# Performance work log

Measured on AMD Instinct MI355X. Metric: run time of the kernel, lower is better.

The kernel has to match this reference:

```python
import jax, jax.numpy as jnp
import numpy as np

NUM_CODES = 4096
TEMPERATURE = 1.0
EPS = 1e-08


def setup_inputs() -> dict:
    key = jax.random.key(0)
    k1, k2, k3 = jax.random.split(key, 3)
    B, D, T = 16, 512, 1500
    encoder_stride = 320
    student_features = jax.random.normal(k1, (B, D, T), dtype=jnp.float32)
    codebook = jax.random.normal(k2, (NUM_CODES, D), dtype=jnp.float32)
    lengths = jax.random.randint(k3, (B,), 0, T * encoder_stride, dtype=jnp.int64)
    return {
        "student_features": student_features,
        "codebook": codebook,
        "lengths": lengths,
        "encoder_stride": encoder_stride,
    }


def _length_mask(lengths, T, stride):
    # frame t is valid iff t < floor(length / stride)  -> (B, T) float mask
    n_valid = jnp.minimum(lengths // stride, T)
    return (jnp.arange(T)[None, :] < n_valid[:, None]).astype(jnp.float32)


def reference(student_features, codebook, lengths, encoder_stride):
    B, D, T = student_features.shape
    mask = _length_mask(lengths, T, encoder_stride)            # (B, T)
    z = jnp.transpose(student_features, (0, 2, 1)).reshape(-1, D)  # (N, D), N = B*T
    # Euclidean cdist via ||z||^2 + ||c||^2 - 2 z c^T (same as torch.cdist GEMM path)
    z2 = jnp.sum(z * z, axis=-1, keepdims=True)                # (N, 1)
    c2 = jnp.sum(codebook * codebook, axis=-1)                 # (K,)
    d2 = z2 + c2[None, :] - 2.0 * (z @ codebook.T)             # (N, K)
    distances = jnp.sqrt(jnp.maximum(d2, 1e-12))
    logits = -distances / TEMPERATURE
    probs = jax.nn.softmax(logits, axis=-1)                    # (N, K)
    probs_masked = probs * mask.reshape(-1, 1)
    code_dist = jnp.sum(probs_masked, axis=0)                  # (K,)
    code_dist = code_dist / (jnp.sum(code_dist) + EPS)
    entropy = -jnp.sum(code_dist * jnp.log(code_dist + EPS))
    max_entropy = jnp.log(jnp.float32(NUM_CODES))
    return 1.0 - entropy / max_entropy
```

## Files before the change

kernel.cpp:

```cpp
#include <hip/hip_runtime.h>
#include <hip/hip_bf16.h>

#define NUM_B   16
#define DIM     512
#define TT      1500
#define NROWS   (NUM_B * TT)
#define NCODES  4096
#define ROW_TILES ((NROWS + 127) / 128)
#define NROWS_PAD (ROW_TILES * 128)
#define NSLICE  8
#define SHIFTC  30.0f

typedef __bf16 bf16x8 __attribute__((ext_vector_type(8)));
typedef float  floatx4 __attribute__((ext_vector_type(4)));
typedef unsigned short ushortx8 __attribute__((ext_vector_type(8)));

__device__ __forceinline__ void glds16(const void* g, void* l) {
    __builtin_amdgcn_global_load_lds(
        (__attribute__((address_space(1))) void*)(void*)g,
        (__attribute__((address_space(3))) void*)l, 16, 0, 0);
}

__global__ __launch_bounds__(256) void k_transpose(
    const float* __restrict__ sf, unsigned short* __restrict__ zbf,
    float* __restrict__ z2) {
    __shared__ float tile[32][68];
    int tid = threadIdx.x;
    int b = blockIdx.z, d0 = blockIdx.y * 64, t0 = blockIdx.x * 32;
    int tl = tid & 31, dg = tid >> 5;
#pragma unroll
    for (int dd = 0; dd < 8; ++dd) {
        int d = dd * 8 + dg;
        int t = t0 + tl;
        if (t < TT) tile[tl][d] = sf[(size_t)(b * DIM + d0 + d) * TT + t];
    }
    __syncthreads();
    int t = tid >> 3, dgrp = tid & 7;
    int tglob = t0 + t;
    float ssq = 0.f;
    if (tglob < TT) {
        unsigned int h[8];
#pragma unroll
        for (int i = 0; i < 8; ++i) {
            __hip_bfloat16 hb = __float2bfloat16(tile[t][dgrp * 8 + i]);
            h[i] = __builtin_bit_cast(unsigned short, hb);
            float vb = __bfloat162float(hb);
            ssq += vb * vb;
        }
        uint4 o;
        o.x = h[0] | (h[1] << 16); o.y = h[2] | (h[3] << 16);
        o.z = h[4] | (h[5] << 16); o.w = h[6] | (h[7] << 16);
        *(uint4*)(zbf + (size_t)(b * TT + tglob) * DIM + d0 + dgrp * 8) = o;
    }
    ssq += __shfl_xor(ssq, 1); ssq += __shfl_xor(ssq, 2); ssq += __shfl_xor(ssq, 4);
    if (dgrp == 0 && tglob < TT) atomicAdd(&z2[b * TT + tglob], ssq);
}

__global__ void k_cb(const float* __restrict__ cb, unsigned short* __restrict__ cbbf,
                     float* __restrict__ c2) {
    int k = blockIdx.x * 4 + (threadIdx.x >> 6);
    int lane = threadIdx.x & 63;
    const float4* src = (const float4*)(cb + (size_t)k * DIM + lane * 8);
    float4 a = src[0], b2 = src[1];
    float vals[8] = {a.x, a.y, a.z, a.w, b2.x, b2.y, b2.z, b2.w};
    float s = 0.f;
    unsigned int h[8];
#pragma unroll
    for (int i = 0; i < 8; ++i) {
        __hip_bfloat16 hb = __float2bfloat16(vals[i]);
        h[i] = __builtin_bit_cast(unsigned short, hb);
        float vb = __bfloat162float(hb);
        s += vb * vb;
    }
    uint4 o;
    o.x = h[0] | (h[1] << 16); o.y = h[2] | (h[3] << 16);
    o.z = h[4] | (h[5] << 16); o.w = h[6] | (h[7] << 16);
    *(uint4*)(cbbf + (size_t)k * DIM + lane * 8) = o;
#pragma unroll
    for (int off = 32; off >= 1; off >>= 1) s += __shfl_down(s, off);
    if (lane == 0) c2[k] = s;
}

__global__ __launch_bounds__(256, 2) void k_gemm1(
    const unsigned short* __restrict__ zbf, const unsigned short* __restrict__ cbbf,
    const float* __restrict__ z2, const float* __restrict__ c2,
    const int* __restrict__ lengths, const int* __restrict__ stride_p,
    float* __restrict__ Sg, unsigned short* __restrict__ Eg) {
    __shared__ unsigned short As[128 * 64];
    __shared__ unsigned short Bs[128 * 64];
    __shared__ float z2s[128], c2s[128];
    __shared__ unsigned char vldp[128];
    __shared__ int s_any;
    int tid = threadIdx.x;
    int r0 = blockIdx.y * 128, c0 = blockIdx.x * 128;
    if (tid == 0) s_any = 0;
    __syncthreads();
    if (tid < 128) {
        int n = r0 + tid;
        int valid = 0;
        if (n < NROWS) {
            int b = n / TT, t = n - b * TT;
            int stride = stride_p[0];
            int nv = lengths[b] / stride;
            if (nv > TT) nv = TT;
            valid = (t < nv);
        }
        if (valid) atomicOr(&s_any, 1);
        vldp[tid] = (unsigned char)valid;
        z2s[tid] = z2[r0 + tid];
        c2s[tid] = c2[c0 + tid];
    }
    __syncthreads();
    if (!s_any) return;

    int wave = tid >> 6, lane = tid & 63;
    int l15 = lane & 15, l4 = lane >> 4;
    int wr = (wave >> 1) * 64, wc = (wave & 1) * 64;

    int srow = lane >> 3;
    int scg = (lane & 7) ^ srow;
    const unsigned short* ag = zbf + (size_t)(r0 + wave * 32 + srow) * DIM + scg * 8;
    const unsigned short* bg = cbbf + (size_t)(c0 + wave * 32 + srow) * DIM + scg * 8;
    unsigned short* al = As + (wave * 32) * 64;
    unsigned short* bl = Bs + (wave * 32) * 64;

    floatx4 acc[4][4];
    const floatx4 zero = {0.f, 0.f, 0.f, 0.f};
#pragma unroll
    for (int i = 0; i < 4; ++i)
#pragma unroll
        for (int j = 0; j < 4; ++j) acc[i][j] = zero;

    int sw = l15 & 7;

    for (int kc = 0; kc < 8; ++kc) {
#pragma unroll
        for (int q = 0; q < 4; ++q) {
            glds16(ag + (size_t)q * 8 * DIM + kc * 64, al + q * 8 * 64);
            glds16(bg + (size_t)q * 8 * DIM + kc * 64, bl + q * 8 * 64);
        }
        __syncthreads();
#pragma unroll
        for (int ks = 0; ks < 64; ks += 32) {
            int g = (ks >> 3) + l4;
            int pcg = g ^ sw;
            bf16x8 av[4], bv[4];
#pragma unroll
            for (int i = 0; i < 4; ++i)
                av[i] = __builtin_bit_cast(bf16x8,
                    *(const ushortx8*)&As[(wr + 16 * i + l15) * 64 + pcg * 8]);
#pragma unroll
            for (int j = 0; j < 4; ++j)
                bv[j] = __builtin_bit_cast(bf16x8,
                    *(const ushortx8*)&Bs[(wc + 16 * j + l15) * 64 + pcg * 8]);
#pragma unroll
            for (int i = 0; i < 4; ++i)
#pragma unroll
                for (int j = 0; j < 4; ++j)
                    acc[i][j] = __builtin_amdgcn_mfma_f32_16x16x32_bf16(av[i], bv[j], acc[i][j], 0, 0, 0);
        }
        __syncthreads();
    }

#pragma unroll
    for (int i = 0; i < 4; ++i) {
#pragma unroll
        for (int r = 0; r < 4; ++r) {
            int rl = wr + 16 * i + 4 * l4 + r;
            bool rv = vldp[rl] != 0;
            float z2v = z2s[rl];
            float s = 0.f;
            unsigned short* Ep = Eg + (size_t)(r0 + rl) * NCODES + c0 + wc + l15;
#pragma unroll
            for (int j = 0; j < 4; ++j) {
                int cl = wc + 16 * j + l15;
                float d2 = z2v + c2s[cl] - 2.0f * acc[i][j][r];
                float d = sqrtf(fmaxf(d2, 1e-12f));
                float e = __expf(SHIFTC - d);
                s += e;
                if (rv) Ep[16 * j] = __builtin_bit_cast(unsigned short, __float2bfloat16(e));
            }
            s += __shfl_xor(s, 1); s += __shfl_xor(s, 2);
            s += __shfl_xor(s, 4); s += __shfl_xor(s, 8);
            if (l15 == 0 && rv) atomicAdd(&Sg[r0 + rl], s);
        }
    }
}

__global__ __launch_bounds__(256) void k_scan(
    const unsigned short* __restrict__ Eg, const float* __restrict__ Sg,
    const int* __restrict__ lengths, const int* __restrict__ stride_p,
    float* __restrict__ cdp) {
    __shared__ float rs[32];
    __shared__ int s_any;
    int tid = threadIdx.x;
    int r0 = blockIdx.y * 32;
    if (tid == 0) s_any = 0;
    __syncthreads();
    if (tid < 32) {
        int n = r0 + tid;
        int valid = 0;
        if (n < NROWS) {
            int b = n / TT, t = n - b * TT;
            int nv = lengths[b] / stride_p[0];
            if (nv > TT) nv = TT;
            valid = (t < nv);
        }
        if (valid) atomicOr(&s_any, 1);
        rs[tid] = valid ? 1.0f / Sg[n] : 0.0f;
    }
    __syncthreads();
    if (!s_any) return;

    int col0 = blockIdx.x * 2048 + tid * 8;
    float acc[8] = {0.f, 0.f, 0.f, 0.f, 0.f, 0.f, 0.f, 0.f};
    for (int nn = 0; nn < 32; ++nn) {
        float rn = rs[nn];
        if (rn == 0.f) continue;
        uint4 v = *(const uint4*)(Eg + (size_t)(r0 + nn) * NCODES + col0);
        unsigned int u[4] = {v.x, v.y, v.z, v.w};
#pragma unroll
        for (int q = 0; q < 4; ++q) {
            acc[2 * q]     += rn * __builtin_bit_cast(float, u[q] << 16);
            acc[2 * q + 1] += rn * __builtin_bit_cast(float, u[q] & 0xffff0000u);
        }
    }
    float* outp = cdp + (size_t)(blockIdx.y & (NSLICE - 1)) * NCODES;
#pragma unroll
    for (int t = 0; t < 8; ++t) atomicAdd(&outp[col0 + t], acc[t]);
}

template <int PASS>
__global__ __launch_bounds__(256, 2) void k_gemm(
    const unsigned short* __restrict__ zbf, const unsigned short* __restrict__ cbbf,
    const float* __restrict__ z2, const float* __restrict__ c2,
    const int* __restrict__ lengths, const int* __restrict__ stride_p,
    float* __restrict__ Sg, float* __restrict__ cd) {
    __shared__ unsigned short As[128 * 64];
    __shared__ unsigned short Bs[128 * 64];
    __shared__ float z2s[128], c2s[128], rs[128];
    __shared__ int s_any;
    int tid = threadIdx.x;
    int r0 = blockIdx.y * 128, c0 = blockIdx.x * 128;
    if (tid == 0) s_any = 0;
    __syncthreads();
    if (tid < 128) {
        int n = r0 + tid;
        int valid = 0;
        if (n < NROWS) {
            int b = n / TT, t = n - b * TT;
            int stride = stride_p[0];
            int nv = lengths[b] / stride;
            if (nv > TT) nv = TT;
            valid = (t < nv);
        }
        if (valid) atomicOr(&s_any, 1);
        z2s[tid] = z2[r0 + tid];
        c2s[tid] = c2[c0 + tid];
        if (PASS == 2) rs[tid] = valid ? (1.0f / Sg[r0 + tid]) : 0.0f;
    }
    __syncthreads();
    if (!s_any) return;

    int wave = tid >> 6, lane = tid & 63;
    int l15 = lane & 15, l4 = lane >> 4;
    int wr = (wave >> 1) * 64, wc = (wave & 1) * 64;
    int srow = lane >> 3;
    int scg = (lane & 7) ^ srow;
    const unsigned short* ag = zbf + (size_t)(r0 + wave * 32 + srow) * DIM + scg * 8;
    const unsigned short* bg = cbbf + (size_t)(c0 + wave * 32 + srow) * DIM + scg * 8;
    unsigned short* al = As + (wave * 32) * 64;
    unsigned short* bl = Bs + (wave * 32) * 64;

    floatx4 acc[4][4];
    const floatx4 zero = {0.f, 0.f, 0.f, 0.f};
#pragma unroll
    for (int i = 0; i < 4; ++i)
#pragma unroll
        for (int j = 0; j < 4; ++j) acc[i][j] = zero;
    int sw = l15 & 7;
    for (int kc = 0; kc < 8; ++kc) {
#pragma unroll
        for (int q = 0; q < 4; ++q) {
            glds16(ag + (size_t)q * 8 * DIM + kc * 64, al + q * 8 * 64);
            glds16(bg + (size_t)q * 8 * DIM + kc * 64, bl + q * 8 * 64);
        }
        __syncthreads();
#pragma unroll
        for (int ks = 0; ks < 64; ks += 32) {
            int g = (ks >> 3) + l4;
            int pcg = g ^ sw;
            bf16x8 av[4], bv[4];
#pragma unroll
            for (int i = 0; i < 4; ++i)
                av[i] = __builtin_bit_cast(bf16x8, *(const ushortx8*)&As[(wr + 16 * i + l15) * 64 + pcg * 8]);
#pragma unroll
            for (int j = 0; j < 4; ++j)
                bv[j] = __builtin_bit_cast(bf16x8, *(const ushortx8*)&Bs[(wc + 16 * j + l15) * 64 + pcg * 8]);
#pragma unroll
            for (int i = 0; i < 4; ++i)
#pragma unroll
                for (int j = 0; j < 4; ++j)
                    acc[i][j] = __builtin_amdgcn_mfma_f32_16x16x32_bf16(av[i], bv[j], acc[i][j], 0, 0, 0);
        }
        __syncthreads();
    }
    if (PASS == 1) {
#pragma unroll
        for (int i = 0; i < 4; ++i) {
#pragma unroll
            for (int r = 0; r < 4; ++r) {
                int rl = wr + 16 * i + 4 * l4 + r;
                float z2v = z2s[rl];
                float s = 0.f;
#pragma unroll
                for (int j = 0; j < 4; ++j) {
                    int cl = wc + 16 * j + l15;
                    float d2 = z2v + c2s[cl] - 2.0f * acc[i][j][r];
                    float d = sqrtf(fmaxf(d2, 1e-12f));
                    s += __expf(SHIFTC - d);
                }
                s += __shfl_xor(s, 1); s += __shfl_xor(s, 2);
                s += __shfl_xor(s, 4); s += __shfl_xor(s, 8);
                if (l15 == 0) atomicAdd(&Sg[r0 + rl], s);
            }
        }
    } else {
#pragma unroll
        for (int j = 0; j < 4; ++j) {
            int cl = wc + 16 * j + l15;
            float c2v = c2s[cl];
            float cs = 0.f;
#pragma unroll
            for (int i = 0; i < 4; ++i) {
#pragma unroll
                for (int r = 0; r < 4; ++r) {
                    int rl = wr + 16 * i + 4 * l4 + r;
                    float d2 = z2s[rl] + c2v - 2.0f * acc[i][j][r];
                    float d = sqrtf(fmaxf(d2, 1e-12f));
                    cs += __expf(SHIFTC - d) * rs[rl];
                }
            }
            cs += __shfl_xor(cs, 16); cs += __shfl_xor(cs, 32);
            if (l4 == 0) atomicAdd(&cd[c0 + cl], cs);
        }
    }
}

__global__ __launch_bounds__(1024) void k_final(const float* __restrict__ cdp,
                                                float* __restrict__ out) {
    __shared__ float red[16];
    __shared__ float tot_s;
    int tid = threadIdx.x, lane = tid & 63, wave = tid >> 6;
    float vloc[4];
    float t = 0.f;
#pragma unroll
    for (int q = 0; q < 4; ++q) {
        int i = tid + q * 1024;
        float v = 0.f;
#pragma unroll
        for (int s = 0; s < NSLICE; ++s) v += cdp[(size_t)s * NCODES + i];
        vloc[q] = v;
        t += v;
    }
#pragma unroll
    for (int off = 32; off >= 1; off >>= 1) t += __shfl_down(t, off);
    if (lane == 0) red[wave] = t;
    __syncthreads();
    if (tid == 0) {
        float tt = 0.f;
#pragma unroll
        for (int w = 0; w < 16; ++w) tt += red[w];
        tot_s = tt;
    }
    __syncthreads();
    float inv = 1.0f / (tot_s + 1e-8f);
    float e = 0.f;
#pragma unroll
    for (int q = 0; q < 4; ++q) {
        float p = vloc[q] * inv;
        e += p * __logf(p + 1e-8f);
    }
#pragma unroll
    for (int off = 32; off >= 1; off >>= 1) e += __shfl_down(e, off);
    if (lane == 0) red[wave] = e;
    __syncthreads();
    if (tid == 0) {
        float ee = 0.f;
#pragma unroll
        for (int w = 0; w < 16; ++w) ee += red[w];
        out[0] = 1.0f - (-ee) / __logf((float)NCODES);
    }
}

extern "C" void kernel_launch(void* const* d_in, const int* in_sizes, int n_in,
                              void* d_out, int out_size, void* d_ws, size_t ws_size,
                              hipStream_t stream) {
    const float* sf = (const float*)d_in[0];
    const float* cb = (const float*)d_in[1];
    const int* lengths = (const int*)d_in[2];
    const int* stride_p = (const int*)d_in[3];

    float* Sg = (float*)d_ws;
    float* cdp = Sg + NROWS_PAD;
    float* z2 = cdp + (size_t)NSLICE * NCODES;
    float* c2 = z2 + NROWS_PAD;
    unsigned short* zbf = (unsigned short*)(c2 + NCODES);
    unsigned short* cbbf = zbf + (size_t)NROWS_PAD * DIM;
    unsigned short* Eg = cbbf + (size_t)NCODES * DIM;

    size_t base_bytes = (size_t)(2 * NROWS_PAD + NCODES) * 4
                      + (size_t)NSLICE * NCODES * 4
                      + ((size_t)NROWS_PAD * DIM + (size_t)NCODES * DIM) * 2;
    size_t need = base_bytes + (size_t)NROWS_PAD * NCODES * 2;

    hipMemsetAsync(Sg, 0, ((size_t)2 * NROWS_PAD + (size_t)NSLICE * NCODES) * sizeof(float), stream);
    k_transpose<<<dim3((TT + 31) / 32, DIM / 64, NUM_B), 256, 0, stream>>>(sf, zbf, z2);
    k_cb<<<dim3(NCODES / 4), 256, 0, stream>>>(cb, cbbf, c2);
    if (ws_size >= need) {
        k_gemm1<<<dim3(NCODES / 128, ROW_TILES), 256, 0, stream>>>(zbf, cbbf, z2, c2, lengths, stride_p, Sg, Eg);
        k_scan<<<dim3(NCODES / 2048, NROWS_PAD / 32), 256, 0, stream>>>(Eg, Sg, lengths, stride_p, cdp);
    } else {
        k_gemm<1><<<dim3(NCODES / 128, ROW_TILES), 256, 0, stream>>>(zbf, cbbf, z2, c2, lengths, stride_p, Sg, cdp);
        k_gemm<2><<<dim3(NCODES / 128, ROW_TILES), 256, 0, stream>>>(zbf, cbbf, z2, c2, lengths, stride_p, Sg, cdp);
    }
    k_final<<<1, 1024, 0, stream>>>(cdp, (float*)d_out);
}
```

Before: 236.4 us.

## Fuse prep kernels, memset, scan and final reduction into fewer launches

Merges the transpose, codebook conversion and workspace zeroing into a single prep kernel, using a full-D shared tile so z2 is written directly instead of accumulated atomically. The GEMM kernel now has the last block per row tile do the column-sum scan of that tile, and the last block overall compute the entropy. This replaces the separate scan and final kernels via atomic counters. It aims to cut launch overhead and memsets, but it serialises the scan work onto one block per row tile and adds a large 32x513 shared tile that may lower occupancy in the prep kernel.

New measurement: 745.7 us. +215.4%, slower.

```diff
diff --git a/kernel.cpp b/kernel.cpp
--- a/kernel.cpp
+++ b/kernel.cpp
@@ -10,6 +10,11 @@
 #define NROWS_PAD (ROW_TILES * 128)
 #define NSLICE  8
 #define SHIFTC  30.0f
+#define NBLKX   (NCODES / 128)
+#define NBLK    (NBLKX * ROW_TILES)
+#define TBLKS   (NUM_B * 47)
+#define CBLKS   (NCODES / 4)
+#define NZERO   (NROWS_PAD + NSLICE * NCODES + ROW_TILES + 1)
 
 typedef __bf16 bf16x8 __attribute__((ext_vector_type(8)));
 typedef float  floatx4 __attribute__((ext_vector_type(4)));
@@ -21,76 +26,90 @@
         (__attribute__((address_space(3))) void*)l, 16, 0, 0);
 }
 
-__global__ __launch_bounds__(256) void k_transpose(
-    const float* __restrict__ sf, unsigned short* __restrict__ zbf,
-    float* __restrict__ z2) {
-    __shared__ float tile[32][68];
-    int tid = threadIdx.x;
-    int b = blockIdx.z, d0 = blockIdx.y * 64, t0 = blockIdx.x * 32;
-    int tl = tid & 31, dg = tid >> 5;
-#pragma unroll
-    for (int dd = 0; dd < 8; ++dd) {
-        int d = dd * 8 + dg;
+__global__ __launch_bounds__(256) void k_prep(
+    const float* __restrict__ sf, const float* __restrict__ cb,
+    unsigned short* __restrict__ zbf, unsigned short* __restrict__ cbbf,
+    float* __restrict__ z2, float* __restrict__ c2, float* __restrict__ zero0) {
+    int id = blockIdx.x, tid = threadIdx.x;
+    if (id < TBLKS) {
+        __shared__ float tile[32][513];
+        int b = id / 47, t0 = (id % 47) * 32;
+        int tl = tid & 31, dg = tid >> 5;
         int t = t0 + tl;
-        if (t < TT) tile[tl][d] = sf[(size_t)(b * DIM + d0 + d) * TT + t];
-    }
-    __syncthreads();
-    int t = tid >> 3, dgrp = tid & 7;
-    int tglob = t0 + t;
-    float ssq = 0.f;
-    if (tglob < TT) {
+        if (t < TT) {
+            const float* src = sf + (size_t)b * DIM * TT + t;
+#pragma unroll 8
+            for (int k = 0; k < 64; ++k) {
+                int d = dg * 64 + k;
+                tile[tl][d] = src[(size_t)d * TT];
+            }
+        }
+        __syncthreads();
+        int tr = tid >> 3, dgr = tid & 7;
+        int tg = t0 + tr;
+        float ssq = 0.f;
+        if (tg < TT) {
+            unsigned short* dst = zbf + (size_t)(b * TT + tg) * DIM;
+#pragma unroll
+            for (int seg = 0; seg < 8; ++seg) {
+                int d0 = seg * 64 + dgr * 8;
+                unsigned int h[8];
+#pragma unroll
+                for (int i2 = 0; i2 < 8; ++i2) {
+                    __hip_bfloat16 hb = __float2bfloat16(tile[tr][d0 + i2]);
+                    h[i2] = __builtin_bit_cast(unsigned short, hb);
+                    float vb = __bfloat162float(hb);
+                    ssq += vb * vb;
+                }
+                uint4 o;
+                o.x = h[0] | (h[1] << 16); o.y = h[2] | (h[3] << 16);
+                o.z = h[4] | (h[5] << 16); o.w = h[6] | (h[7] << 16);
+                *(uint4*)(dst + d0) = o;
+            }
+        }
+        ssq += __shfl_xor(ssq, 1); ssq += __shfl_xor(ssq, 2); ssq += __shfl_xor(ssq, 4);
+        if (dgr == 0 && tg < TT) z2[b * TT + tg] = ssq;
+    } else {
+        int ci = id - TBLKS;
+        int gid = ci * 256 + tid;
+        if (gid < NZERO) zero0[gid] = 0.f;
+        int k = ci * 4 + (tid >> 6);
+        int lane = tid & 63;
+        const float4* src = (const float4*)(cb + (size_t)k * DIM + lane * 8);
+        float4 a = src[0], b2 = src[1];
+        float vals[8] = {a.x, a.y, a.z, a.w, b2.x, b2.y, b2.z, b2.w};
+        float s = 0.f;
         unsigned int h[8];
 #pragma unroll
         for (int i = 0; i < 8; ++i) {
-            __hip_bfloat16 hb = __float2bfloat16(tile[t][dgrp * 8 + i]);
+            __hip_bfloat16 hb = __float2bfloat16(vals[i]);
             h[i] = __builtin_bit_cast(unsigned short, hb);
             float vb = __bfloat162float(hb);
-            ssq += vb * vb;
+            s += vb * vb;
         }
         uint4 o;
         o.x = h[0] | (h[1] << 16); o.y = h[2] | (h[3] << 16);
         o.z = h[4] | (h[5] << 16); o.w = h[6] | (h[7] << 16);
-        *(uint4*)(zbf + (size_t)(b * TT + tglob) * DIM + d0 + dgrp * 8) = o;
-    }
-    ssq += __shfl_xor(ssq, 1); ssq += __shfl_xor(ssq, 2); ssq += __shfl_xor(ssq, 4);
-    if (dgrp == 0 && tglob < TT) atomicAdd(&z2[b * TT + tglob], ssq);
-}
-
-__global__ void k_cb(const float* __restrict__ cb, unsigned short* __restrict__ cbbf,
-                     float* __restrict__ c2) {
-    int k = blockIdx.x * 4 + (threadIdx.x >> 6);
-    int lane = threadIdx.x & 63;
-    const float4* src = (const float4*)(cb + (size_t)k * DIM + lane * 8);
-    float4 a = src[0], b2 = src[1];
-    float vals[8] = {a.x, a.y, a.z, a.w, b2.x, b2.y, b2.z, b2.w};
-    float s = 0.f;
-    unsigned int h[8];
-#pragma unroll
-    for (int i = 0; i < 8; ++i) {
-        __hip_bfloat16 hb = __float2bfloat16(vals[i]);
-        h[i] = __builtin_bit_cast(unsigned short, hb);
-        float vb = __bfloat162float(hb);
-        s += vb * vb;
-    }
-    uint4 o;
-    o.x = h[0] | (h[1] << 16); o.y = h[2] | (h[3] << 16);
-    o.z = h[4] | (h[5] << 16); o.w = h[6] | (h[7] << 16);
-    *(uint4*)(cbbf + (size_t)k * DIM + lane * 8) = o;
-#pragma unroll
-    for (int off = 32; off >= 1; off >>= 1) s += __shfl_down(s, off);
-    if (lane == 0) c2[k] = s;
+        *(uint4*)(cbbf + (size_t)k * DIM + lane * 8) = o;
+#pragma unroll
+        for (int off = 32; off >= 1; off >>= 1) s += __shfl_down(s, off);
+        if (lane == 0) c2[k] = s;
+    }
 }
 
 __global__ __launch_bounds__(256, 2) void k_gemm1(
     const unsigned short* __restrict__ zbf, const unsigned short* __restrict__ cbbf,
     const float* __restrict__ z2, const float* __restrict__ c2,
     const int* __restrict__ lengths, const int* __restrict__ stride_p,
-    float* __restrict__ Sg, unsigned short* __restrict__ Eg) {
+    float* __restrict__ Sg, unsigned short* __restrict__ Eg,
+    float* __restrict__ cdp, int* __restrict__ rowcnt, int* __restrict__ blockdone,
+    float* __restrict__ out) {
     __shared__ unsigned short As[128 * 64];
     __shared__ unsigned short Bs[128 * 64];
-    __shared__ float z2s[128], c2s[128];
+    __shared__ float z2s[128], c2s[128], rsS[128];
     __shared__ unsigned char vldp[128];
-    __shared__ int s_any;
+    __shared__ int s_any, sh_e;
+    __shared__ float red[4], tot_s;
     int tid = threadIdx.x;
     int r0 = blockIdx.y * 128, c0 = blockIdx.x * 128;
     if (tid == 0) s_any = 0;
@@ -111,123 +130,146 @@
         c2s[tid] = c2[c0 + tid];
     }
     __syncthreads();
-    if (!s_any) return;
-
-    int wave = tid >> 6, lane = tid & 63;
-    int l15 = lane & 15, l4 = lane >> 4;
-    int wr = (wave >> 1) * 64, wc = (wave & 1) * 64;
-
-    int srow = lane >> 3;
-    int scg = (lane & 7) ^ srow;
-    const unsigned short* ag = zbf + (size_t)(r0 + wave * 32 + srow) * DIM + scg * 8;
-    const unsigned short* bg = cbbf + (size_t)(c0 + wave * 32 + srow) * DIM + scg * 8;
-    unsigned short* al = As + (wave * 32) * 64;
-    unsigned short* bl = Bs + (wave * 32) * 64;
-
-    floatx4 acc[4][4];
-    const floatx4 zero = {0.f, 0.f, 0.f, 0.f};
-#pragma unroll
-    for (int i = 0; i < 4; ++i)
-#pragma unroll
-        for (int j = 0; j < 4; ++j) acc[i][j] = zero;
-
-    int sw = l15 & 7;
-
-    for (int kc = 0; kc < 8; ++kc) {
-#pragma unroll
-        for (int q = 0; q < 4; ++q) {
-            glds16(ag + (size_t)q * 8 * DIM + kc * 64, al + q * 8 * 64);
-            glds16(bg + (size_t)q * 8 * DIM + kc * 64, bl + q * 8 * 64);
-        }
-        __syncthreads();
-#pragma unroll
-        for (int ks = 0; ks < 64; ks += 32) {
-            int g = (ks >> 3) + l4;
-            int pcg = g ^ sw;
-            bf16x8 av[4], bv[4];
-#pragma unroll
-            for (int i = 0; i < 4; ++i)
-                av[i] = __builtin_bit_cast(bf16x8,
-                    *(const ushortx8*)&As[(wr + 16 * i + l15) * 64 + pcg * 8]);
-#pragma unroll
-            for (int j = 0; j < 4; ++j)
-                bv[j] = __builtin_bit_cast(bf16x8,
-                    *(const ushortx8*)&Bs[(wc + 16 * j + l15) * 64 + pcg * 8]);
-#pragma unroll
-            for (int i = 0; i < 4; ++i)
+    if (s_any) {
+        int wave = tid >> 6, lane = tid & 63;
+        int l15 = lane & 15, l4 = lane >> 4;
+        int wr = (wave >> 1) * 64, wc = (wave & 1) * 64;
+
+        int srow = lane >> 3;
+        int scg = (lane & 7) ^ srow;
+        const unsigned short* ag = zbf + (size_t)(r0 + wave * 32 + srow) * DIM + scg * 8;
+        const unsigned short* bg = cbbf + (size_t)(c0 + wave * 32 + srow) * DIM + scg * 8;
+        unsigned short* al = As + (wave * 32) * 64;
+        unsigned short* bl = Bs + (wave * 32) * 64;
+
+        floatx4 acc[4][4];
+        const floatx4 zero = {0.f, 0.f, 0.f, 0.f};
+#pragma unroll
+        for (int i = 0; i < 4; ++i)
+#pragma unroll
+            for (int j = 0; j < 4; ++j) acc[i][j] = zero;
+
+        int sw = l15 & 7;
+
+        for (int kc = 0; kc < 8; ++kc) {
+#pragma unroll
+            for (int q = 0; q < 4; ++q) {
+                glds16(ag + (size_t)q * 8 * DIM + kc * 64, al + q * 8 * 64);
+                glds16(bg + (size_t)q * 8 * DIM + kc * 64, bl + q * 8 * 64);
+            }
+            __syncthreads();
+#pragma unroll
+            for (int ks = 0; ks < 64; ks += 32) {
+                int g = (ks >> 3) + l4;
+                int pcg = g ^ sw;
+                bf16x8 av[4], bv[4];
+#pragma unroll
+                for (int i = 0; i < 4; ++i)
+                    av[i] = __builtin_bit_cast(bf16x8,
+                        *(const ushortx8*)&As[(wr + 16 * i + l15) * 64 + pcg * 8]);
 #pragma unroll
                 for (int j = 0; j < 4; ++j)
-                    acc[i][j] = __builtin_amdgcn_mfma_f32_16x16x32_bf16(av[i], bv[j], acc[i][j], 0, 0, 0);
-        }
-        __syncthreads();
-    }
-
-#pragma unroll
-    for (int i = 0; i < 4; ++i) {
-#pragma unroll
-        for (int r = 0; r < 4; ++r) {
-            int rl = wr + 16 * i + 4 * l4 + r;
-            bool rv = vldp[rl] != 0;
-            float z2v = z2s[rl];
-            float s = 0.f;
-            unsigned short* Ep = Eg + (size_t)(r0 + rl) * NCODES + c0 + wc + l15;
-#pragma unroll
-            for (int j = 0; j < 4; ++j) {
-                int cl = wc + 16 * j + l15;
-                float d2 = z2v + c2s[cl] - 2.0f * acc[i][j][r];
-                float d = sqrtf(fmaxf(d2, 1e-12f));
-                float e = __expf(SHIFTC - d);
-                s += e;
-                if (rv) Ep[16 * j] = __builtin_bit_cast(unsigned short, __float2bfloat16(e));
-            }
-            s += __shfl_xor(s, 1); s += __shfl_xor(s, 2);
-            s += __shfl_xor(s, 4); s += __shfl_xor(s, 8);
-            if (l15 == 0 && rv) atomicAdd(&Sg[r0 + rl], s);
-        }
-    }
-}
-
-__global__ __launch_bounds__(256) void k_scan(
-    const unsigned short* __restrict__ Eg, const float* __restrict__ Sg,
-    const int* __restrict__ lengths, const int* __restrict__ stride_p,
-    float* __restrict__ cdp) {
-    __shared__ float rs[32];
-    __shared__ int s_any;
-    int tid = threadIdx.x;
-    int r0 = blockIdx.y * 32;
-    if (tid == 0) s_any = 0;
-    __syncthreads();
-    if (tid < 32) {
-        int n = r0 + tid;
-        int valid = 0;
-        if (n < NROWS) {
-            int b = n / TT, t = n - b * TT;
-            int nv = lengths[b] / stride_p[0];
-            if (nv > TT) nv = TT;
-            valid = (t < nv);
-        }
-        if (valid) atomicOr(&s_any, 1);
-        rs[tid] = valid ? 1.0f / Sg[n] : 0.0f;
-    }
-    __syncthreads();
-    if (!s_any) return;
-
-    int col0 = blockIdx.x * 2048 + tid * 8;
-    float acc[8] = {0.f, 0.f, 0.f, 0.f, 0.f, 0.f, 0.f, 0.f};
-    for (int nn = 0; nn < 32; ++nn) {
-        float rn = rs[nn];
-        if (rn == 0.f) continue;
-        uint4 v = *(const uint4*)(Eg + (size_t)(r0 + nn) * NCODES + col0);
-        unsigned int u[4] = {v.x, v.y, v.z, v.w};
-#pragma unroll
-        for (int q = 0; q < 4; ++q) {
-            acc[2 * q]     += rn * __builtin_bit_cast(float, u[q] << 16);
-            acc[2 * q + 1] += rn * __builtin_bit_cast(float, u[q] & 0xffff0000u);
-        }
-    }
-    float* outp = cdp + (size_t)(blockIdx.y & (NSLICE - 1)) * NCODES;
-#pragma unroll
-    for (int t = 0; t < 8; ++t) atomicAdd(&outp[col0 + t], acc[t]);
+                    bv[j] = __builtin_bit_cast(bf16x8,
+                        *(const ushortx8*)&Bs[(wc + 16 * j + l15) * 64 + pcg * 8]);
+#pragma unroll
+                for (int i = 0; i < 4; ++i)
+#pragma unroll
+                    for (int j = 0; j < 4; ++j)
+                        acc[i][j] = __builtin_amdgcn_mfma_f32_16x16x32_bf16(av[i], bv[j], acc[i][j], 0, 0, 0);
+            }
+            __syncthreads();
+        }
+
+#pragma unroll
+        for (int i = 0; i < 4; ++i) {
+#pragma unroll
+            for (int r = 0; r < 4; ++r) {
+                int rl = wr + 16 * i + 4 * l4 + r;
+                bool rv = vldp[rl] != 0;
+                float z2v = z2s[rl];
+                float s = 0.f;
+                unsigned short* Ep = Eg + (size_t)(r0 + rl) * NCODES + c0 + wc + l15;
+#pragma unroll
+                for (int j = 0; j < 4; ++j) {
+                    int cl = wc + 16 * j + l15;
+                    float d2 = z2v + c2s[cl] - 2.0f * acc[i][j][r];
+                    float d = sqrtf(fmaxf(d2, 1e-12f));
+                    float e = __expf(SHIFTC - d);
+                    s += e;
+                    if (rv) Ep[16 * j] = __builtin_bit_cast(unsigned short, __float2bfloat16(e));
+                }
+                s += __shfl_xor(s, 1); s += __shfl_xor(s, 2);
+                s += __shfl_xor(s, 4); s += __shfl_xor(s, 8);
+                if (l15 == 0 && rv) atomicAdd(&Sg[r0 + rl], s);
+            }
+        }
+
+        __threadfence();
+        __syncthreads();
+        if (tid == 0) sh_e = (atomicAdd(&rowcnt[blockIdx.y], 1) == NBLKX - 1);
+        __syncthreads();
+        if (sh_e) {
+            if (tid < 128) rsS[tid] = vldp[tid] ? 1.0f / Sg[r0 + tid] : 0.0f;
+            __syncthreads();
+            float* outp = cdp + (size_t)(blockIdx.y & (NSLICE - 1)) * NCODES;
+#pragma unroll
+            for (int half = 0; half < 2; ++half) {
+                int col0 = half * 2048 + tid * 8;
+                float a[8] = {0.f, 0.f, 0.f, 0.f, 0.f, 0.f, 0.f, 0.f};
+                for (int nn = 0; nn < 128; ++nn) {
+                    float rn = rsS[nn];
+                    if (rn == 0.f) continue;
+                    uint4 v = *(const uint4*)(Eg + (size_t)(r0 + nn) * NCODES + col0);
+                    unsigned int u[4] = {v.x, v.y, v.z, v.w};
+#pragma unroll
+                    for (int q = 0; q < 4; ++q) {
+                        a[2 * q]     += rn * __builtin_bit_cast(float, u[q] << 16);
+                        a[2 * q + 1] += rn * __builtin_bit_cast(float, u[q] & 0xffff0000u);
+                    }
+                }
+#pragma unroll
+                for (int q = 0; q < 8; ++q) atomicAdd(&outp[col0 + q], a[q]);
+            }
+            __threadfence();
+        }
+    }
+    __syncthreads();
+    if (tid == 0) sh_e = (atomicAdd(blockdone, 1) == NBLK - 1);
+    __syncthreads();
+    if (sh_e) {
+        float vloc[16];
+        float tsum = 0.f;
+#pragma unroll
+        for (int q = 0; q < 16; ++q) {
+            int i = q * 256 + tid;
+            float v = 0.f;
+#pragma unroll
+            for (int s = 0; s < NSLICE; ++s) v += cdp[(size_t)s * NCODES + i];
+            vloc[q] = v;
+            tsum += v;
+        }
+#pragma unroll
+        for (int off = 32; off >= 1; off >>= 1) tsum += __shfl_down(tsum, off);
+        if ((tid & 63) == 0) red[tid >> 6] = tsum;
+        __syncthreads();
+        if (tid == 0) tot_s = red[0] + red[1] + red[2] + red[3];
+        __syncthreads();
+        float inv = 1.0f / (tot_s + 1e-8f);
+        float e = 0.f;
+#pragma unroll
+        for (int q = 0; q < 16; ++q) {
+            float p = vloc[q] * inv;
+            e += p * __logf(p + 1e-8f);
+        }
+#pragma unroll
+        for (int off = 32; off >= 1; off >>= 1) e += __shfl_down(e, off);
+        if ((tid & 63) == 0) red[tid >> 6] = e;
+        __syncthreads();
+        if (tid == 0) {
+            float ee = red[0] + red[1] + red[2] + red[3];
+            out[0] = 1.0f - (-ee) / __logf((float)NCODES);
+        }
+    }
 }
 
 template <int PASS>
@@ -401,28 +443,32 @@
     const int* lengths = (const int*)d_in[2];
     const int* stride_p = (const int*)d_in[3];
 
-    float* Sg = (float*)d_ws;
+    float* wsf = (float*)d_ws;
+    float* Sg = wsf;
     float* cdp = Sg + NROWS_PAD;
-    float* z2 = cdp + (size_t)NSLICE * NCODES;
-    float* c2 = z2 + NROWS_PAD;
-    unsigned short* zbf = (unsigned short*)(c2 + NCODES);
+    int* rowcnt = (int*)(cdp + (size_t)NSLICE * NCODES);
+    int* blockdone = rowcnt + ROW_TILES;
+    const size_t OFF_Z2 = NZERO;
+    const size_t OFF_C2 = OFF_Z2 + NROWS_PAD;
+    const size_t OFF_ZB = (OFF_C2 + NCODES + 3) & ~(size_t)3;
+    float* z2 = wsf + OFF_Z2;
+    float* c2 = wsf + OFF_C2;
+    unsigned short* zbf = (unsigned short*)(wsf + OFF_ZB);
     unsigned short* cbbf = zbf + (size_t)NROWS_PAD * DIM;
     unsigned short* Eg = cbbf + (size_t)NCODES * DIM;
 
-    size_t base_bytes = (size_t)(2 * NROWS_PAD + NCODES) * 4
-                      + (size_t)NSLICE * NCODES * 4
-                      + ((size_t)NROWS_PAD * DIM + (size_t)NCODES * DIM) * 2;
-    size_t need = base_bytes + (size_t)NROWS_PAD * NCODES * 2;
-
-    hipMemsetAsync(Sg, 0, ((size_t)2 * NROWS_PAD + (size_t)NSLICE * NCODES) * sizeof(float), stream);
-    k_transpose<<<dim3((TT + 31) / 32, DIM / 64, NUM_B), 256, 0, stream>>>(sf, zbf, z2);
-    k_cb<<<dim3(NCODES / 4), 256, 0, stream>>>(cb, cbbf, c2);
+    size_t need = OFF_ZB * 4
+                + ((size_t)NROWS_PAD * DIM + (size_t)NCODES * DIM
+                 + (size_t)NROWS_PAD * NCODES) * 2;
+
+    k_prep<<<dim3(TBLKS + CBLKS), 256, 0, stream>>>(sf, cb, zbf, cbbf, z2, c2, Sg);
     if (ws_size >= need) {
-        k_gemm1<<<dim3(NCODES / 128, ROW_TILES), 256, 0, stream>>>(zbf, cbbf, z2, c2, lengths, stride_p, Sg, Eg);
-        k_scan<<<dim3(NCODES / 2048, NROWS_PAD / 32), 256, 0, stream>>>(Eg, Sg, lengths, stride_p, cdp);
+        k_gemm1<<<dim3(NBLKX, ROW_TILES), 256, 0, stream>>>(
+            zbf, cbbf, z2, c2, lengths, stride_p, Sg, Eg, cdp, rowcnt, blockdone,
+            (float*)d_out);
     } else {
-        k_gemm<1><<<dim3(NCODES / 128, ROW_TILES), 256, 0, stream>>>(zbf, cbbf, z2, c2, lengths, stride_p, Sg, cdp);
-        k_gemm<2><<<dim3(NCODES / 128, ROW_TILES), 256, 0, stream>>>(zbf, cbbf, z2, c2, lengths, stride_p, Sg, cdp);
-    }
-    k_final<<<1, 1024, 0, stream>>>(cdp, (float*)d_out);
-}
+        k_gemm<1><<<dim3(NBLKX, ROW_TILES), 256, 0, stream>>>(zbf, cbbf, z2, c2, lengths, stride_p, Sg, cdp);
+        k_gemm<2><<<dim3(NBLKX, ROW_TILES), 256, 0, stream>>>(zbf, cbbf, z2, c2, lengths, stride_p, Sg, cdp);
+        k_final<<<1, 1024, 0, stream>>>(cdp, (float*)d_out);
+    }
+}
```
